# Performance work log

Hardware: AMD Instinct MI355X
Metric: run time of the kernel (lower is better)

## Reference

```python
import jax, jax.numpy as jnp
import numpy as np

N_NODES = 50000
N_EDGES = 200000
IN_DIM = 512
HID = 2000
LAT = 128


def setup_inputs() -> dict:
    key = jax.random.key(0)
    ks = jax.random.split(key, 6)
    x = jax.random.normal(ks[0], (N_NODES, IN_DIM), dtype=jnp.float32)
    edge_index = jax.random.randint(ks[1], (2, N_EDGES), 0, N_NODES, dtype=jnp.int64)
    # glorot-ish scales so ReLU/Sigmoid stay in a sane range
    W1 = jax.random.normal(ks[2], (IN_DIM, HID), dtype=jnp.float32) * (1.0 / np.sqrt(IN_DIM))
    b1 = jnp.zeros((HID,), dtype=jnp.float32)
    W2 = jax.random.normal(ks[3], (HID, LAT), dtype=jnp.float32) * (1.0 / np.sqrt(HID))
    b2 = jnp.zeros((LAT,), dtype=jnp.float32)
    return {"x": x, "edge_index": edge_index, "W1": W1, "b1": b1, "W2": W2, "b2": b2}


def gcn_conv(x, edge_index, W, b):
    """PyG GCNConv: D^-1/2 (A+I) D^-1/2 (X W) + b, unit edge weights."""
    n = x.shape[0]
    loops = jnp.arange(n, dtype=edge_index.dtype)
    row = jnp.concatenate([edge_index[0], loops])  # source nodes
    col = jnp.concatenate([edge_index[1], loops])  # target nodes
    deg = jax.ops.segment_sum(jnp.ones_like(col, dtype=x.dtype), col, num_segments=n)
    dis = jnp.where(deg > 0, jax.lax.rsqrt(deg), 0.0)  # deg^-1/2, inf -> 0
    norm = dis[row] * dis[col]                         # [E+N]
    h = x @ W                                          # transform first: [N, out]
    msg = h[row] * norm[:, None]                       # gather + normalize: [E+N, out]
    out = jax.ops.segment_sum(msg, col, num_segments=n)  # scatter-add
    return out + b


def reference(x, edge_index, W1, b1, W2, b2):
    h = jax.nn.relu(gcn_conv(x, edge_index, W1, b1))
    return jax.nn.sigmoid(gcn_conv(h, edge_index, W2, b2))
```

## Files before the change

### kernel.cpp

```cpp
#include <hip/hip_runtime.h>
#include <hip/hip_fp16.h>

#define NN 50000
#define NE 200000
#define IND 512
#define HIDD 2000
#define LATD 128

#define M_PAD 50048
#define N1_PAD 2048
#define MT1 391
#define NT1 16
#define SLAB1 49

typedef _Float16 f16x8 __attribute__((ext_vector_type(8)));
typedef float f32x4 __attribute__((ext_vector_type(4)));

__device__ __forceinline__ void gload_lds16(const _Float16* g, _Float16* l) {
    __builtin_amdgcn_global_load_lds(
        (const __attribute__((address_space(1))) unsigned int*)g,
        (__attribute__((address_space(3))) unsigned int*)l,
        16, 0, 0);
}

__global__ void k_degree(const int* __restrict__ col, int* __restrict__ deg) {
    int e = blockIdx.x * 256 + threadIdx.x;
    if (e < NE) atomicAdd(&deg[col[e]], 1);
}

__global__ void k_dis(const int* __restrict__ deg, float* __restrict__ dis) {
    int i = blockIdx.x * 256 + threadIdx.x;
    if (i < NN) dis[i] = rsqrtf((float)deg[i] + 1.0f);
}

__global__ void k_scan(const int* __restrict__ deg, int* __restrict__ row_ptr) {
    __shared__ int smem[1024];
    const int tid = threadIdx.x;
    int carry = 0;
    for (int chunk = 0; chunk < NN; chunk += 1024) {
        int i = chunk + tid;
        int v = (i < NN) ? deg[i] : 0;
        smem[tid] = v;
        __syncthreads();
        #pragma unroll
        for (int off = 1; off < 1024; off <<= 1) {
            int t = (tid >= off) ? smem[tid - off] : 0;
            __syncthreads();
            if (tid >= off) smem[tid] += t;
            __syncthreads();
        }
        if (i < NN) row_ptr[i] = carry + smem[tid] - v;
        int tot = smem[1023];
        __syncthreads();
        carry += tot;
    }
    if (tid == 0) row_ptr[NN] = carry;
}

__global__ void k_fill(const int* __restrict__ ei, const int* __restrict__ row_ptr,
                       int* __restrict__ cursor, int* __restrict__ csr_src) {
    int e = blockIdx.x * 256 + threadIdx.x;
    if (e < NE) {
        int r = ei[e], c = ei[NE + e];
        int pos = atomicAdd(&cursor[c], 1);
        csr_src[row_ptr[c] + pos] = r;
    }
}

__global__ void k_transpose_tiled(const float* __restrict__ in,
                                  _Float16* __restrict__ out, int R, int C, int ldo) {
    __shared__ float sm[32][33];
    int c0 = blockIdx.x * 32, r0 = blockIdx.y * 32;
    int tx = threadIdx.x & 31, ty = threadIdx.x >> 5;
    #pragma unroll
    for (int i = 0; i < 4; ++i) {
        int r = r0 + ty + i * 8, c = c0 + tx;
        sm[ty + i * 8][tx] = (r < R && c < C) ? in[(size_t)r * C + c] : 0.f;
    }
    __syncthreads();
    #pragma unroll
    for (int i = 0; i < 4; ++i) {
        int c = c0 + ty + i * 8, r = r0 + tx;
        if (c < C && r < R) out[(size_t)c * ldo + r] = (_Float16)sm[tx][ty + i * 8];
    }
}

__global__ void k_gather_x(const float* __restrict__ x, const int* __restrict__ row_ptr,
                           const int* __restrict__ csr_src, const float* __restrict__ dis,
                           _Float16* __restrict__ Ah) {
    int dst = blockIdx.x * 4 + (threadIdx.x >> 6);
    if (dst >= NN) return;
    int lane = threadIdx.x & 63;
    float dd = dis[dst];
    const float* xd = x + (size_t)dst * IND + lane * 8;
    float4 a0 = *(const float4*)xd;
    float4 a1 = *(const float4*)(xd + 4);
    float acc[8] = { dd*a0.x, dd*a0.y, dd*a0.z, dd*a0.w,
                     dd*a1.x, dd*a1.y, dd*a1.z, dd*a1.w };
    int beg = row_ptr[dst], end = row_ptr[dst + 1];
    for (int i = beg; i < end; ++i) {
        int s = csr_src[i];
        float ns = dis[s];
        const float* xs = x + (size_t)s * IND + lane * 8;
        float4 b0 = *(const float4*)xs;
        float4 b1 = *(const float4*)(xs + 4);
        acc[0] += ns * b0.x; acc[1] += ns * b0.y; acc[2] += ns * b0.z; acc[3] += ns * b0.w;
        acc[4] += ns * b1.x; acc[5] += ns * b1.y; acc[6] += ns * b1.z; acc[7] += ns * b1.w;
    }
    f16x8 o;
    #pragma unroll
    for (int i = 0; i < 8; ++i) o[i] = (_Float16)(dd * acc[i]);
    *(f16x8*)(Ah + (size_t)dst * IND + lane * 8) = o;
}

__global__ void k_gather_t(const float* __restrict__ t, const int* __restrict__ row_ptr,
                           const int* __restrict__ csr_src, const float* __restrict__ dis,
                           const float* __restrict__ b2, float* __restrict__ out) {
    int dst = blockIdx.x * 4 + (threadIdx.x >> 6);
    if (dst >= NN) return;
    int lane = threadIdx.x & 63;
    float dd = dis[dst];
    float2 td = *(const float2*)(t + (size_t)dst * LATD + lane * 2);
    float accx = dd * td.x, accy = dd * td.y;
    int beg = row_ptr[dst], end = row_ptr[dst + 1];
    for (int i = beg; i < end; ++i) {
        int s = csr_src[i];
        float ns = dis[s];
        float2 ts = *(const float2*)(t + (size_t)s * LATD + lane * 2);
        accx += ns * ts.x; accy += ns * ts.y;
    }
    float2 bb = *(const float2*)(b2 + lane * 2);
    float vx = dd * accx + bb.x;
    float vy = dd * accy + bb.y;
    float2 o;
    o.x = 1.0f / (1.0f + __expf(-vx));
    o.y = 1.0f / (1.0f + __expf(-vy));
    *(float2*)(out + (size_t)dst * LATD + lane * 2) = o;
}

__global__ __launch_bounds__(256, 2) void k_gemm1(
    const _Float16* __restrict__ A,
    const _Float16* __restrict__ Bt,
    const float* __restrict__ bias,
    _Float16* __restrict__ Ch)
{
    const int b = blockIdx.x;
    const int mT = (b & 7) * SLAB1 + ((b >> 3) >> 4);
    const int nT = (b >> 3) & 15;
    if (mT >= MT1) return;
    const int mBase = mT * 128;
    const int nBase = nT * 128;

    __shared__ __align__(16) _Float16 As[128 * 32];
    __shared__ __align__(16) _Float16 Bs[128 * 32];

    const int tid = threadIdx.x;
    const int lane = tid & 63;
    const int w = tid >> 6;

    const int srow = w * 32 + (lane >> 2);
    const int scol = (lane & 3) * 8;
    const _Float16* Ag0 = A + (size_t)(mBase + srow) * IND + scol;
    const _Float16* Ag1 = Ag0 + (size_t)16 * IND;
    const _Float16* Bg0 = Bt + (size_t)(nBase + srow) * IND + scol;
    const _Float16* Bg1 = Bg0 + (size_t)16 * IND;
    _Float16* Asl0 = As + w * 1024;
    _Float16* Asl1 = Asl0 + 512;
    _Float16* Bsl0 = Bs + w * 1024;
    _Float16* Bsl1 = Bsl0 + 512;

    const int wm = (w >> 1) * 64;
    const int wn = (w & 1) * 64;
    const int lm = lane & 15;
    const int quad = lane >> 4;

    f32x4 acc[4][4];
    #pragma unroll
    for (int i = 0; i < 4; ++i)
        #pragma unroll
        for (int j = 0; j < 4; ++j)
            acc[i][j] = (f32x4){0.f, 0.f, 0.f, 0.f};

    for (int k0 = 0; k0 < IND; k0 += 32) {
        gload_lds16(Ag0 + k0, Asl0);
        gload_lds16(Ag1 + k0, Asl1);
        gload_lds16(Bg0 + k0, Bsl0);
        gload_lds16(Bg1 + k0, Bsl1);
        __syncthreads();

        f16x8 af[4], bfr[4];
        #pragma unroll
        for (int mi = 0; mi < 4; ++mi)
            af[mi] = *(const f16x8*)&As[(wm + mi * 16 + lm) * 32 + quad * 8];
        #pragma unroll
        for (int ni = 0; ni < 4; ++ni)
            bfr[ni] = *(const f16x8*)&Bs[(wn + ni * 16 + lm) * 32 + quad * 8];
        #pragma unroll
        for (int mi = 0; mi < 4; ++mi)
            #pragma unroll
            for (int ni = 0; ni < 4; ++ni)
                acc[mi][ni] = __builtin_amdgcn_mfma_f32_16x16x32_f16(
                    af[mi], bfr[ni], acc[mi][ni], 0, 0, 0);
        __syncthreads();
    }

    #pragma unroll
    for (int mi = 0; mi < 4; ++mi) {
        #pragma unroll
        for (int ni = 0; ni < 4; ++ni) {
            int col = nBase + wn + ni * 16 + lm;
            float bval = bias[col];
            #pragma unroll
            for (int r = 0; r < 4; ++r) {
                int rowg = mBase + wm + mi * 16 + quad * 4 + r;
                float v = fmaxf(acc[mi][ni][r] + bval, 0.f);
                Ch[(size_t)rowg * N1_PAD + col] = (_Float16)v;
            }
        }
    }
}

__global__ __launch_bounds__(256, 2) void k_gemm2(
    const _Float16* __restrict__ A,
    const _Float16* __restrict__ Bt,
    float* __restrict__ Cf)
{
    __shared__ __align__(16) _Float16 As[64 * 32];
    __shared__ __align__(16) _Float16 Bs[128 * 32];

    const int tid = threadIdx.x;
    const int lane = tid & 63;
    const int w = tid >> 6;
    const int mBase = blockIdx.x * 64;

    const int srA = w * 16 + (lane >> 2);
    const int srB = w * 32 + (lane >> 2);
    const int scol = (lane & 3) * 8;
    const _Float16* Ag  = A + (size_t)(mBase + srA) * N1_PAD + scol;
    const _Float16* Bg0 = Bt + (size_t)srB * N1_PAD + scol;
    const _Float16* Bg1 = Bg0 + (size_t)16 * N1_PAD;
    _Float16* Asl  = As + w * 512;
    _Float16* Bsl0 = Bs + w * 1024;
    _Float16* Bsl1 = Bsl0 + 512;

    const int wm = (w & 1) * 32;
    const int wn = (w >> 1) * 64;
    const int lm = lane & 15;
    const int quad = lane >> 4;

    f32x4 acc[2][4];
    #pragma unroll
    for (int i = 0; i < 2; ++i)
        #pragma unroll
        for (int j = 0; j < 4; ++j)
            acc[i][j] = (f32x4){0.f, 0.f, 0.f, 0.f};

    for (int k0 = 0; k0 < N1_PAD; k0 += 32) {
        gload_lds16(Ag + k0, Asl);
        gload_lds16(Bg0 + k0, Bsl0);
        gload_lds16(Bg1 + k0, Bsl1);
        __syncthreads();

        f16x8 af[2], bfr[4];
        #pragma unroll
        for (int mi = 0; mi < 2; ++mi)
            af[mi] = *(const f16x8*)&As[(wm + mi * 16 + lm) * 32 + quad * 8];
        #pragma unroll
        for (int ni = 0; ni < 4; ++ni)
            bfr[ni] = *(const f16x8*)&Bs[(wn + ni * 16 + lm) * 32 + quad * 8];
        #pragma unroll
        for (int mi = 0; mi < 2; ++mi)
            #pragma unroll
            for (int ni = 0; ni < 4; ++ni)
                acc[mi][ni] = __builtin_amdgcn_mfma_f32_16x16x32_f16(
                    af[mi], bfr[ni], acc[mi][ni], 0, 0, 0);
        __syncthreads();
    }

    #pragma unroll
    for (int mi = 0; mi < 2; ++mi) {
        #pragma unroll
        for (int ni = 0; ni < 4; ++ni) {
            int col = wn + ni * 16 + lm;
            #pragma unroll
            for (int r = 0; r < 4; ++r) {
                int rowg = mBase + wm + mi * 16 + quad * 4 + r;
                Cf[(size_t)rowg * LATD + col] = acc[mi][ni][r];
            }
        }
    }
}

extern "C" void kernel_launch(void* const* d_in, const int* in_sizes, int n_in,
                              void* d_out, int out_size, void* d_ws, size_t ws_size,
                              hipStream_t stream) {
    const float* x  = (const float*)d_in[0];
    const int* ei   = (const int*)d_in[1];
    const float* W1 = (const float*)d_in[2];
    const float* b1 = (const float*)d_in[3];
    const float* W2 = (const float*)d_in[4];
    const float* b2 = (const float*)d_in[5];
    float* out = (float*)d_out;

    char* p = (char*)d_ws;
    auto alloc = [&](size_t bytes) {
        char* q = p; p += (bytes + 255) & ~(size_t)255; return q;
    };
    int* deg        = (int*)alloc((size_t)NN * 4);
    int* row_ptr    = (int*)alloc((size_t)(NN + 1) * 4);
    int* cursor     = (int*)alloc((size_t)NN * 4);
    int* csr_src    = (int*)alloc((size_t)NE * 4);
    float* dis      = (float*)alloc((size_t)NN * 4);
    float* b1pad    = (float*)alloc((size_t)N1_PAD * 4);
    _Float16* W1T   = (_Float16*)alloc((size_t)N1_PAD * IND * 2);
    _Float16* W2T   = (_Float16*)alloc((size_t)LATD * N1_PAD * 2);
    _Float16* Ah    = (_Float16*)alloc((size_t)M_PAD * IND * 2);
    _Float16* h     = (_Float16*)alloc((size_t)M_PAD * N1_PAD * 2);
    float* t        = (float*)alloc((size_t)M_PAD * LATD * 4);

    hipMemsetAsync(deg,    0, (size_t)NN * 4, stream);
    hipMemsetAsync(cursor, 0, (size_t)NN * 4, stream);
    hipMemsetAsync(b1pad,  0, (size_t)N1_PAD * 4, stream);
    hipMemsetAsync(W1T,    0, (size_t)N1_PAD * IND * 2, stream);
    hipMemsetAsync(W2T,    0, (size_t)LATD * N1_PAD * 2, stream);
    hipMemcpyAsync(b1pad, b1, (size_t)HIDD * 4, hipMemcpyDeviceToDevice, stream);

    k_degree<<<(NE + 255) / 256, 256, 0, stream>>>(ei + NE, deg);
    k_dis<<<(NN + 255) / 256, 256, 0, stream>>>(deg, dis);
    k_scan<<<1, 1024, 0, stream>>>(deg, row_ptr);
    k_fill<<<(NE + 255) / 256, 256, 0, stream>>>(ei, row_ptr, cursor, csr_src);

    {
        dim3 gt1((HIDD + 31) / 32, (IND + 31) / 32);
        k_transpose_tiled<<<gt1, 256, 0, stream>>>(W1, W1T, IND, HIDD, IND);
        dim3 gt2((LATD + 31) / 32, (HIDD + 31) / 32);
        k_transpose_tiled<<<gt2, 256, 0, stream>>>(W2, W2T, HIDD, LATD, N1_PAD);
    }

    k_gather_x<<<(NN + 3) / 4, 256, 0, stream>>>(x, row_ptr, csr_src, dis, Ah);

    k_gemm1<<<8 * SLAB1 * NT1, 256, 0, stream>>>(Ah, W1T, b1pad, h);
    k_gemm2<<<M_PAD / 64, 256, 0, stream>>>(h, W2T, t);

    k_gather_t<<<(NN + 3) / 4, 256, 0, stream>>>(t, row_ptr, csr_src, dis, b2, out);
}
```

Measured before the change: 597.1 us.

## Parallelize CSR scan, pre-convert x to fp16, and double K-step in GEMMs

Replaces the single-block serial prefix scan with a three-kernel block-sum, block-scan and final-scan. Adds a pass that converts x to fp16 so the neighbour gather reads half the bytes per row. Both GEMMs now load two 32-wide K slices per barrier pair, halving the number of syncs at the cost of doubled LDS usage. The fp16 pre-conversion adds a full extra read and write of x, and the larger LDS footprint may lower occupancy.

```diff
diff --git a/kernel.cpp b/kernel.cpp
--- a/kernel.cpp
+++ b/kernel.cpp
@@ -10,8 +10,8 @@
 #define M_PAD 50048
 #define N1_PAD 2048
 #define MT1 391
-#define NT1 16
 #define SLAB1 49
+#define NBLK 196
 
 typedef _Float16 f16x8 __attribute__((ext_vector_type(8)));
 typedef float f32x4 __attribute__((ext_vector_type(4)));
@@ -33,28 +33,50 @@
     if (i < NN) dis[i] = rsqrtf((float)deg[i] + 1.0f);
 }
 
-__global__ void k_scan(const int* __restrict__ deg, int* __restrict__ row_ptr) {
-    __shared__ int smem[1024];
-    const int tid = threadIdx.x;
-    int carry = 0;
-    for (int chunk = 0; chunk < NN; chunk += 1024) {
-        int i = chunk + tid;
-        int v = (i < NN) ? deg[i] : 0;
-        smem[tid] = v;
-        __syncthreads();
-        #pragma unroll
-        for (int off = 1; off < 1024; off <<= 1) {
-            int t = (tid >= off) ? smem[tid - off] : 0;
-            __syncthreads();
-            if (tid >= off) smem[tid] += t;
-            __syncthreads();
-        }
-        if (i < NN) row_ptr[i] = carry + smem[tid] - v;
-        int tot = smem[1023];
-        __syncthreads();
-        carry += tot;
-    }
-    if (tid == 0) row_ptr[NN] = carry;
+__global__ void k_bsum(const int* __restrict__ deg, int* __restrict__ bsum) {
+    __shared__ int sm[4];
+    int i = blockIdx.x * 256 + threadIdx.x;
+    int v = (i < NN) ? deg[i] : 0;
+    #pragma unroll
+    for (int off = 32; off; off >>= 1) v += __shfl_down(v, off, 64);
+    if ((threadIdx.x & 63) == 0) sm[threadIdx.x >> 6] = v;
+    __syncthreads();
+    if (threadIdx.x == 0) bsum[blockIdx.x] = sm[0] + sm[1] + sm[2] + sm[3];
+}
+
+__global__ void k_bscan(int* __restrict__ bsum) {
+    __shared__ int sm[256];
+    int tid = threadIdx.x;
+    int v = (tid < NBLK) ? bsum[tid] : 0;
+    sm[tid] = v;
+    __syncthreads();
+    #pragma unroll
+    for (int off = 1; off < 256; off <<= 1) {
+        int t = (tid >= off) ? sm[tid - off] : 0;
+        __syncthreads();
+        sm[tid] += t;
+        __syncthreads();
+    }
+    if (tid < NBLK) bsum[tid] = sm[tid] - v;
+}
+
+__global__ void k_scan_final(const int* __restrict__ deg, const int* __restrict__ bsum,
+                             int* __restrict__ row_ptr) {
+    __shared__ int sm[256];
+    int b = blockIdx.x, tid = threadIdx.x;
+    int i = b * 256 + tid;
+    int v = (i < NN) ? deg[i] : 0;
+    sm[tid] = v;
+    __syncthreads();
+    #pragma unroll
+    for (int off = 1; off < 256; off <<= 1) {
+        int t = (tid >= off) ? sm[tid - off] : 0;
+        __syncthreads();
+        sm[tid] += t;
+        __syncthreads();
+    }
+    if (i < NN) row_ptr[i] = bsum[b] + sm[tid] - v;
+    if (i == NN - 1) row_ptr[NN] = bsum[b] + sm[tid];
 }
 
 __global__ void k_fill(const int* __restrict__ ei, const int* __restrict__ row_ptr,
@@ -85,27 +107,36 @@
     }
 }
 
-__global__ void k_gather_x(const float* __restrict__ x, const int* __restrict__ row_ptr,
+__global__ void k_xcvt(const float* __restrict__ in, _Float16* __restrict__ out, int n8) {
+    int i = blockIdx.x * 256 + threadIdx.x;
+    if (i < n8) {
+        float4 a = ((const float4*)in)[i * 2];
+        float4 b = ((const float4*)in)[i * 2 + 1];
+        f16x8 o;
+        o[0] = (_Float16)a.x; o[1] = (_Float16)a.y; o[2] = (_Float16)a.z; o[3] = (_Float16)a.w;
+        o[4] = (_Float16)b.x; o[5] = (_Float16)b.y; o[6] = (_Float16)b.z; o[7] = (_Float16)b.w;
+        ((f16x8*)out)[i] = o;
+    }
+}
+
+__global__ void k_gather_x(const _Float16* __restrict__ xh, const int* __restrict__ row_ptr,
                            const int* __restrict__ csr_src, const float* __restrict__ dis,
                            _Float16* __restrict__ Ah) {
     int dst = blockIdx.x * 4 + (threadIdx.x >> 6);
     if (dst >= NN) return;
     int lane = threadIdx.x & 63;
     float dd = dis[dst];
-    const float* xd = x + (size_t)dst * IND + lane * 8;
-    float4 a0 = *(const float4*)xd;
-    float4 a1 = *(const float4*)(xd + 4);
-    float acc[8] = { dd*a0.x, dd*a0.y, dd*a0.z, dd*a0.w,
-                     dd*a1.x, dd*a1.y, dd*a1.z, dd*a1.w };
+    f16x8 sv = *(const f16x8*)(xh + (size_t)dst * IND + lane * 8);
+    float acc[8];
+    #pragma unroll
+    for (int i = 0; i < 8; ++i) acc[i] = dd * (float)sv[i];
     int beg = row_ptr[dst], end = row_ptr[dst + 1];
     for (int i = beg; i < end; ++i) {
         int s = csr_src[i];
         float ns = dis[s];
-        const float* xs = x + (size_t)s * IND + lane * 8;
-        float4 b0 = *(const float4*)xs;
-        float4 b1 = *(const float4*)(xs + 4);
-        acc[0] += ns * b0.x; acc[1] += ns * b0.y; acc[2] += ns * b0.z; acc[3] += ns * b0.w;
-        acc[4] += ns * b1.x; acc[5] += ns * b1.y; acc[6] += ns * b1.z; acc[7] += ns * b1.w;
+        f16x8 v = *(const f16x8*)(xh + (size_t)s * IND + lane * 8);
+        #pragma unroll
+        for (int q = 0; q < 8; ++q) acc[q] += ns * (float)v[q];
     }
     f16x8 o;
     #pragma unroll
@@ -151,8 +182,8 @@
     const int mBase = mT * 128;
     const int nBase = nT * 128;
 
-    __shared__ __align__(16) _Float16 As[128 * 32];
-    __shared__ __align__(16) _Float16 Bs[128 * 32];
+    __shared__ __align__(16) _Float16 As[2 * 128 * 32];
+    __shared__ __align__(16) _Float16 Bs[2 * 128 * 32];
 
     const int tid = threadIdx.x;
     const int lane = tid & 63;
@@ -164,10 +195,6 @@
     const _Float16* Ag1 = Ag0 + (size_t)16 * IND;
     const _Float16* Bg0 = Bt + (size_t)(nBase + srow) * IND + scol;
     const _Float16* Bg1 = Bg0 + (size_t)16 * IND;
-    _Float16* Asl0 = As + w * 1024;
-    _Float16* Asl1 = Asl0 + 512;
-    _Float16* Bsl0 = Bs + w * 1024;
-    _Float16* Bsl1 = Bsl0 + 512;
 
     const int wm = (w >> 1) * 64;
     const int wn = (w & 1) * 64;
@@ -181,26 +208,32 @@
         for (int j = 0; j < 4; ++j)
             acc[i][j] = (f32x4){0.f, 0.f, 0.f, 0.f};
 
-    for (int k0 = 0; k0 < IND; k0 += 32) {
-        gload_lds16(Ag0 + k0, Asl0);
-        gload_lds16(Ag1 + k0, Asl1);
-        gload_lds16(Bg0 + k0, Bsl0);
-        gload_lds16(Bg1 + k0, Bsl1);
-        __syncthreads();
-
-        f16x8 af[4], bfr[4];
-        #pragma unroll
-        for (int mi = 0; mi < 4; ++mi)
-            af[mi] = *(const f16x8*)&As[(wm + mi * 16 + lm) * 32 + quad * 8];
-        #pragma unroll
-        for (int ni = 0; ni < 4; ++ni)
-            bfr[ni] = *(const f16x8*)&Bs[(wn + ni * 16 + lm) * 32 + quad * 8];
-        #pragma unroll
-        for (int mi = 0; mi < 4; ++mi)
+    for (int k0 = 0; k0 < IND; k0 += 64) {
+        #pragma unroll
+        for (int s = 0; s < 2; ++s) {
+            gload_lds16(Ag0 + k0 + s * 32, As + s * 4096 + w * 1024);
+            gload_lds16(Ag1 + k0 + s * 32, As + s * 4096 + w * 1024 + 512);
+            gload_lds16(Bg0 + k0 + s * 32, Bs + s * 4096 + w * 1024);
+            gload_lds16(Bg1 + k0 + s * 32, Bs + s * 4096 + w * 1024 + 512);
+        }
+        __syncthreads();
+
+        #pragma unroll
+        for (int s = 0; s < 2; ++s) {
+            f16x8 af[4], bfr[4];
+            #pragma unroll
+            for (int mi = 0; mi < 4; ++mi)
+                af[mi] = *(const f16x8*)&As[s * 4096 + (wm + mi * 16 + lm) * 32 + quad * 8];
             #pragma unroll
             for (int ni = 0; ni < 4; ++ni)
-                acc[mi][ni] = __builtin_amdgcn_mfma_f32_16x16x32_f16(
-                    af[mi], bfr[ni], acc[mi][ni], 0, 0, 0);
+                bfr[ni] = *(const f16x8*)&Bs[s * 4096 + (wn + ni * 16 + lm) * 32 + quad * 8];
+            #pragma unroll
+            for (int mi = 0; mi < 4; ++mi)
+                #pragma unroll
+                for (int ni = 0; ni < 4; ++ni)
+                    acc[mi][ni] = __builtin_amdgcn_mfma_f32_16x16x32_f16(
+                        af[mi], bfr[ni], acc[mi][ni], 0, 0, 0);
+        }
         __syncthreads();
     }
 
@@ -225,8 +258,8 @@
     const _Float16* __restrict__ Bt,
     float* __restrict__ Cf)
 {
-    __shared__ __align__(16) _Float16 As[64 * 32];
-    __shared__ __align__(16) _Float16 Bs[128 * 32];
+    __shared__ __align__(16) _Float16 As[2 * 64 * 32];
+    __shared__ __align__(16) _Float16 Bs[2 * 128 * 32];
 
     const int tid = threadIdx.x;
     const int lane = tid & 63;
@@ -239,9 +272,6 @@
     const _Float16* Ag  = A + (size_t)(mBase + srA) * N1_PAD + scol;
     const _Float16* Bg0 = Bt + (size_t)srB * N1_PAD + scol;
     const _Float16* Bg1 = Bg0 + (size_t)16 * N1_PAD;
-    _Float16* Asl  = As + w * 512;
-    _Float16* Bsl0 = Bs + w * 1024;
-    _Float16* Bsl1 = Bsl0 + 512;
 
     const int wm = (w & 1) * 32;
     const int wn = (w >> 1) * 64;
@@ -255,25 +285,31 @@
         for (int j = 0; j < 4; ++j)
             acc[i][j] = (f32x4){0.f, 0.f, 0.f, 0.f};
 
-    for (int k0 = 0; k0 < N1_PAD; k0 += 32) {
-        gload_lds16(Ag + k0, Asl);
-        gload_lds16(Bg0 + k0, Bsl0);
-        gload_lds16(Bg1 + k0, Bsl1);
-        __syncthreads();
-
-        f16x8 af[2], bfr[4];
-        #pragma unroll
-        for (int mi = 0; mi < 2; ++mi)
-            af[mi] = *(const f16x8*)&As[(wm + mi * 16 + lm) * 32 + quad * 8];
-        #pragma unroll
-        for (int ni = 0; ni < 4; ++ni)
-            bfr[ni] = *(const f16x8*)&Bs[(wn + ni * 16 + lm) * 32 + quad * 8];
-        #pragma unroll
-        for (int mi = 0; mi < 2; ++mi)
+    for (int k0 = 0; k0 < N1_PAD; k0 += 64) {
+        #pragma unroll
+        for (int s = 0; s < 2; ++s) {
+            gload_lds16(Ag + k0 + s * 32, As + s * 2048 + w * 512);
+            gload_lds16(Bg0 + k0 + s * 32, Bs + s * 4096 + w * 1024);
+            gload_lds16(Bg1 + k0 + s * 32, Bs + s * 4096 + w * 1024 + 512);
+        }
+        __syncthreads();
+
+        #pragma unroll
+        for (int s = 0; s < 2; ++s) {
+            f16x8 af[2], bfr[4];
+            #pragma unroll
+            for (int mi = 0; mi < 2; ++mi)
+                af[mi] = *(const f16x8*)&As[s * 2048 + (wm + mi * 16 + lm) * 32 + quad * 8];
             #pragma unroll
             for (int ni = 0; ni < 4; ++ni)
-                acc[mi][ni] = __builtin_amdgcn_mfma_f32_16x16x32_f16(
-                    af[mi], bfr[ni], acc[mi][ni], 0, 0, 0);
+                bfr[ni] = *(const f16x8*)&Bs[s * 4096 + (wn + ni * 16 + lm) * 32 + quad * 8];
+            #pragma unroll
+            for (int mi = 0; mi < 2; ++mi)
+                #pragma unroll
+                for (int ni = 0; ni < 4; ++ni)
+                    acc[mi][ni] = __builtin_amdgcn_mfma_f32_16x16x32_f16(
+                        af[mi], bfr[ni], acc[mi][ni], 0, 0, 0);
+        }
         __syncthreads();
     }
 
@@ -307,6 +343,7 @@
         char* q = p; p += (bytes + 255) & ~(size_t)255; return q;
     };
     int* deg        = (int*)alloc((size_t)NN * 4);
+    int* bsum       = (int*)alloc((size_t)NBLK * 4);
     int* row_ptr    = (int*)alloc((size_t)(NN + 1) * 4);
     int* cursor     = (int*)alloc((size_t)NN * 4);
     int* csr_src    = (int*)alloc((size_t)NE * 4);
@@ -314,6 +351,7 @@
     float* b1pad    = (float*)alloc((size_t)N1_PAD * 4);
     _Float16* W1T   = (_Float16*)alloc((size_t)N1_PAD * IND * 2);
     _Float16* W2T   = (_Float16*)alloc((size_t)LATD * N1_PAD * 2);
+    _Float16* xh    = (_Float16*)alloc((size_t)NN * IND * 2);
     _Float16* Ah    = (_Float16*)alloc((size_t)M_PAD * IND * 2);
     _Float16* h     = (_Float16*)alloc((size_t)M_PAD * N1_PAD * 2);
     float* t        = (float*)alloc((size_t)M_PAD * LATD * 4);
@@ -327,7 +365,9 @@
 
     k_degree<<<(NE + 255) / 256, 256, 0, stream>>>(ei + NE, deg);
     k_dis<<<(NN + 255) / 256, 256, 0, stream>>>(deg, dis);
-    k_scan<<<1, 1024, 0, stream>>>(deg, row_ptr);
+    k_bsum<<<NBLK, 256, 0, stream>>>(deg, bsum);
+    k_bscan<<<1, 256, 0, stream>>>(bsum);
+    k_scan_final<<<NBLK, 256, 0, stream>>>(deg, bsum, row_ptr);
     k_fill<<<(NE + 255) / 256, 256, 0, stream>>>(ei, row_ptr, cursor, csr_src);
 
     {
@@ -335,11 +375,12 @@
         k_transpose_tiled<<<gt1, 256, 0, stream>>>(W1, W1T, IND, HIDD, IND);
         dim3 gt2((LATD + 31) / 32, (HIDD + 31) / 32);
         k_transpose_tiled<<<gt2, 256, 0, stream>>>(W2, W2T, HIDD, LATD, N1_PAD);
-    }
-
-    k_gather_x<<<(NN + 3) / 4, 256, 0, stream>>>(x, row_ptr, csr_src, dis, Ah);
-
-    k_gemm1<<<8 * SLAB1 * NT1, 256, 0, stream>>>(Ah, W1T, b1pad, h);
+        k_xcvt<<<(NN * IND / 8 + 255) / 256, 256, 0, stream>>>(x, xh, NN * IND / 8);
+    }
+
+    k_gather_x<<<(NN + 3) / 4, 256, 0, stream>>>(xh, row_ptr, csr_src, dis, Ah);
+
+    k_gemm1<<<8 * SLAB1 * 16, 256, 0, stream>>>(Ah, W1T, b1pad, h);
     k_gemm2<<<M_PAD / 64, 256, 0, stream>>>(h, W2T, t);
 
     k_gather_t<<<(NN + 3) / 4, 256, 0, stream>>>(t, row_ptr, csr_src, dis, b2, out);
```

New measurement: 506.3 us. -15.2%, faster.
